# Optimization experiments

Measured on AMD Instinct MI355X. Metric: run time of the kernel, lower is better.

Reference implementation:

```python
import jax, jax.numpy as jnp
import numpy as np

NPOS_MAX = 64
SCALE = 0.125  # head_dim ** -0.5


def setup_inputs() -> dict:
    key = jax.random.key(0)
    kq, kk, kv, kp, kw = jax.random.split(key, 5)
    B, S, D = 32, 1024, 64
    return {
        "q": jax.random.normal(kq, (B, S, D), dtype=jnp.float32),
        "k": jax.random.normal(kk, (B, S, D), dtype=jnp.float32),
        "v": jax.random.normal(kv, (B, S, D), dtype=jnp.float32),
        "pos_emb": jax.random.normal(kp, (1, D, NPOS_MAX), dtype=jnp.float32) * 0.02,
        "w_k": jax.random.normal(kw, (1, D, D), dtype=jnp.float32) * 0.02,
        "is_cope_k": 1,
    }


def reference(q, k, v, pos_emb, w_k, is_cope_k):
    # mode == 0: plain scaled QK^T
    attn_logits = jnp.einsum("bqd,bkd->bqk", q * SCALE, k)  # [B,S,S]
    gates = jax.nn.sigmoid(attn_logits)
    # reverse cumulative sum along the key axis (flip-cumsum-flip)
    pos = jnp.cumsum(gates[..., ::-1], axis=-1)[..., ::-1]
    pos = jnp.minimum(pos, NPOS_MAX - 1)
    pos_ceil = jnp.ceil(pos).astype(jnp.int32)
    pos_floor = jnp.floor(pos).astype(jnp.int32)
    base = q if is_cope_k else k
    logits_int = jnp.einsum("bsd,odn->bsn", base, pos_emb)  # [B,S,npos]
    logits_ceil = jnp.take_along_axis(logits_int, pos_ceil, axis=-1)
    logits_floor = jnp.take_along_axis(logits_int, pos_floor, axis=-1)
    w = pos - pos_floor.astype(pos.dtype)
    return logits_ceil * w + logits_floor * (1.0 - w)
```

## Files before the change

### kernel.cpp

```cpp
#include <hip/hip_runtime.h>

#define SLEN 1024
#define DDIM 64
#define NPOS 64
#define QROWS 16
#define QCOLS 256
#define COPE_SCALE 0.125f
#define GSTR 260
#define TSTR 66

typedef __bf16 bf16x8 __attribute__((ext_vector_type(8)));
typedef float f32x4 __attribute__((ext_vector_type(4)));

__device__ __forceinline__ unsigned short f2bf_hi(float x) {
    unsigned u = __builtin_bit_cast(unsigned, x);
    unsigned r = u + 0x7FFFu + ((u >> 16) & 1u);
    return (unsigned short)(r >> 16);
}
__device__ __forceinline__ float bf2f(unsigned short h) {
    unsigned u = ((unsigned)h) << 16;
    return __builtin_bit_cast(float, u);
}
struct U8 { ushort4 a, b; };
__device__ __forceinline__ bf16x8 pack8(const unsigned short* s) {
    U8 u = {{s[0], s[1], s[2], s[3]}, {s[4], s[5], s[6], s[7]}};
    return __builtin_bit_cast(bf16x8, u);
}

__global__ __launch_bounds__(256) void prep_kernel(
    const float* __restrict__ k,
    unsigned short* __restrict__ khi,
    unsigned short* __restrict__ klo,
    int n4)
{
    int i = blockIdx.x * 256 + threadIdx.x;
    if (i >= n4) return;
    float4 v = ((const float4*)k)[i];
    ushort4 h, l;
    h.x = f2bf_hi(v.x); l.x = f2bf_hi(v.x - bf2f(h.x));
    h.y = f2bf_hi(v.y); l.y = f2bf_hi(v.y - bf2f(h.y));
    h.z = f2bf_hi(v.z); l.z = f2bf_hi(v.z - bf2f(h.z));
    h.w = f2bf_hi(v.w); l.w = f2bf_hi(v.w - bf2f(h.w));
    ((ushort4*)khi)[i] = h;
    ((ushort4*)klo)[i] = l;
}

__global__ __launch_bounds__(256, 6) void cope_mfma_kernel(
    const float* __restrict__ q,
    const float* __restrict__ k,
    const float* __restrict__ pos_emb,
    const int*   __restrict__ is_cope_k,
    const unsigned short* __restrict__ khi,
    const unsigned short* __restrict__ klo,
    float*       __restrict__ out)
{
    __shared__ __align__(16) float G[QROWS * GSTR];
    __shared__ __align__(16) float tableL[QROWS * TSTR];
    __shared__ float Racc[QROWS];

    const int t = threadIdx.x;
    const int wave = t >> 6;
    const int lane = t & 63;
    const int quad = lane >> 4;
    const int nloc = lane & 15;
    const int blk = blockIdx.x;
    const int batch = blk >> 6;
    const int qbase = (blk & 63) * QROWS;

    if (t < QROWS) Racc[t] = 0.f;

    bf16x8 a_hi[2], a_lo[2];
    {
        const float* qrow = q + (size_t)(batch * SLEN + qbase + nloc) * DDIM + quad * 8;
        #pragma unroll
        for (int ks = 0; ks < 2; ++ks) {
            float4 v0 = *(const float4*)(qrow + ks * 32);
            float4 v1 = *(const float4*)(qrow + ks * 32 + 4);
            float xs[8] = {v0.x, v0.y, v0.z, v0.w, v1.x, v1.y, v1.z, v1.w};
            unsigned short hb[8], lb[8];
            #pragma unroll
            for (int j = 0; j < 8; ++j) {
                hb[j] = f2bf_hi(xs[j]);
                lb[j] = f2bf_hi(xs[j] - bf2f(hb[j]));
            }
            a_hi[ks] = pack8(hb);
            a_lo[ks] = pack8(lb);
        }
    }

    {
        const int icope = *is_cope_k;
        bf16x8 t_hi[2], t_lo[2];
        if (icope) {
            t_hi[0] = a_hi[0]; t_hi[1] = a_hi[1];
            t_lo[0] = a_lo[0]; t_lo[1] = a_lo[1];
        } else {
            size_t boff = (size_t)(batch * SLEN + qbase + nloc) * DDIM + quad * 8;
            t_hi[0] = __builtin_bit_cast(bf16x8, *(const uint4*)(khi + boff));
            t_hi[1] = __builtin_bit_cast(bf16x8, *(const uint4*)(khi + boff + 32));
            t_lo[0] = __builtin_bit_cast(bf16x8, *(const uint4*)(klo + boff));
            t_lo[1] = __builtin_bit_cast(bf16x8, *(const uint4*)(klo + boff + 32));
        }
        bf16x8 p_hi[2];
        #pragma unroll
        for (int ks = 0; ks < 2; ++ks) {
            unsigned short hb[8];
            #pragma unroll
            for (int j = 0; j < 8; ++j) {
                float pv = pos_emb[(quad * 8 + j + ks * 32) * NPOS + wave * 16 + nloc];
                hb[j] = f2bf_hi(pv);
            }
            p_hi[ks] = pack8(hb);
        }
        f32x4 tacc = {0.f, 0.f, 0.f, 0.f};
        tacc = __builtin_amdgcn_mfma_f32_16x16x32_bf16(t_hi[0], p_hi[0], tacc, 0, 0, 0);
        tacc = __builtin_amdgcn_mfma_f32_16x16x32_bf16(t_lo[0], p_hi[0], tacc, 0, 0, 0);
        tacc = __builtin_amdgcn_mfma_f32_16x16x32_bf16(t_hi[1], p_hi[1], tacc, 0, 0, 0);
        tacc = __builtin_amdgcn_mfma_f32_16x16x32_bf16(t_lo[1], p_hi[1], tacc, 0, 0, 0);
        #pragma unroll
        for (int reg = 0; reg < 4; ++reg)
            tableL[(quad * 4 + reg) * TSTR + wave * 16 + nloc] = tacc[reg];
    }

    int remaining = 0;
    for (int qi = 3; qi >= 0; --qi) {
        #pragma unroll
        for (int i = 0; i < 4; ++i) {
            const int tl = wave * 4 + i;
            size_t boff = (size_t)(batch * SLEN + qi * QCOLS + tl * 16 + nloc) * DDIM + quad * 8;
            uint4 bh0 = *(const uint4*)(khi + boff);
            uint4 bh1 = *(const uint4*)(khi + boff + 32);
            uint4 bl0 = *(const uint4*)(klo + boff);
            uint4 bl1 = *(const uint4*)(klo + boff + 32);
            f32x4 acc = {0.f, 0.f, 0.f, 0.f};
            acc = __builtin_amdgcn_mfma_f32_16x16x32_bf16(a_hi[0], __builtin_bit_cast(bf16x8, bh0), acc, 0, 0, 0);
            acc = __builtin_amdgcn_mfma_f32_16x16x32_bf16(a_lo[0], __builtin_bit_cast(bf16x8, bh0), acc, 0, 0, 0);
            acc = __builtin_amdgcn_mfma_f32_16x16x32_bf16(a_hi[0], __builtin_bit_cast(bf16x8, bl0), acc, 0, 0, 0);
            acc = __builtin_amdgcn_mfma_f32_16x16x32_bf16(a_hi[1], __builtin_bit_cast(bf16x8, bh1), acc, 0, 0, 0);
            acc = __builtin_amdgcn_mfma_f32_16x16x32_bf16(a_lo[1], __builtin_bit_cast(bf16x8, bh1), acc, 0, 0, 0);
            acc = __builtin_amdgcn_mfma_f32_16x16x32_bf16(a_hi[1], __builtin_bit_cast(bf16x8, bl1), acc, 0, 0, 0);
            #pragma unroll
            for (int reg = 0; reg < 4; ++reg) {
                float x = acc[reg] * COPE_SCALE;
                float g = __builtin_amdgcn_rcpf(1.0f + __expf(-x));
                G[(quad * 4 + reg) * GSTR + tl * 16 + nloc] = g;
            }
        }
        __syncthreads();

        #pragma unroll
        for (int rep = 0; rep < 4; ++rep) {
            const int row = wave * 4 + rep;
            const float roff = Racc[row];
            float4 gv = *(const float4*)&G[row * GSTR + lane * 4];
            float ls3 = gv.w;
            float ls2 = gv.z + ls3;
            float ls1 = gv.y + ls2;
            float ls0 = gv.x + ls1;
            const float T = ls0;
            float v = T;
            #pragma unroll
            for (int ofs = 1; ofs < 64; ofs <<= 1) {
                float u = __shfl_down(v, ofs);
                if (lane + ofs < 64) v += u;
            }
            if (lane == 0) Racc[row] = roff + v;
            const float E = (v - T) + roff;

            const float tabv = tableL[row * TSTR + lane];
            float dtabv = __shfl_down(tabv, 1) - tabv;
            if (lane == 63) dtabv = 0.f;
            float ls[4] = {ls0, ls1, ls2, ls3};
            float res[4];
            #pragma unroll
            for (int i = 0; i < 4; ++i) {
                float p = ls[i] + E;
                p = fminf(p, (float)(NPOS - 1));
                float pf = floorf(p);
                int fi = (int)pf;
                float w = p - pf;
                float tf = __shfl(tabv, fi);
                float td = __shfl(dtabv, fi);
                res[i] = tf + w * td;
            }
            float* orow = out + (size_t)(batch * SLEN + qbase + row) * SLEN + qi * QCOLS + lane * 4;
            f32x4 o = {res[0], res[1], res[2], res[3]};
            __builtin_nontemporal_store(o, (f32x4*)orow);
        }
        __syncthreads();

        float mn = Racc[0];
        #pragma unroll
        for (int r = 1; r < QROWS; ++r) mn = fminf(mn, Racc[r]);
        if (mn >= (float)(NPOS - 1)) { remaining = qi; break; }
    }

    if (remaining > 0) {
        const int ncols = remaining * QCOLS;
        #pragma unroll
        for (int rep = 0; rep < 4; ++rep) {
            const int row = wave * 4 + rep;
            const float v63 = tableL[row * TSTR + (NPOS - 1)];
            f32x4 bv = {v63, v63, v63, v63};
            float* orow = out + (size_t)(batch * SLEN + qbase + row) * SLEN;
            for (int c = lane * 4; c < ncols; c += 256)
                __builtin_nontemporal_store(bv, (f32x4*)(orow + c));
        }
    }
}

#define KTILE 128
#define KPAD 68
#define NTILES (SLEN / KTILE)
#define FQROWS 8

__global__ __launch_bounds__(256) void cope_fallback(
    const float* __restrict__ q,
    const float* __restrict__ k,
    const float* __restrict__ pos_emb,
    const int*   __restrict__ is_cope_k,
    float*       __restrict__ out)
{
    __shared__ __align__(16) float smem[KTILE * KPAD];
    __shared__ __align__(16) float qT[DDIM][FQROWS];
    __shared__ __align__(16) float baseT[DDIM][FQROWS];
    __shared__ __align__(16) float tableL2[FQROWS][NPOS];

    const int t = threadIdx.x;
    const int blk = blockIdx.x;
    const int batch = blk / (SLEN / FQROWS);
    const int qbase = (blk % (SLEN / FQROWS)) * FQROWS;
    const float* bsrc = (*is_cope_k) ? q : k;

    for (int i = t; i < FQROWS * DDIM; i += 256) {
        int r = i >> 6, d = i & 63;
        size_t gi = (size_t)(batch * SLEN + qbase + r) * DDIM + d;
        qT[d][r] = q[gi];
        baseT[d][r] = bsrc[gi];
    }
    __syncthreads();
    for (int i = t; i < FQROWS * NPOS; i += 256) {
        int r = i >> 6, n = i & 63;
        float a = 0.f;
        #pragma unroll
        for (int d = 0; d < DDIM; ++d) a += baseT[d][r] * pos_emb[d * NPOS + n];
        tableL2[r][n] = a;
    }
    const int jl = t & 127;
    const int qg = t >> 7;
    float acc[4][NTILES];
    #pragma unroll
    for (int r = 0; r < 4; ++r)
        #pragma unroll
        for (int tl = 0; tl < NTILES; ++tl) acc[r][tl] = 0.f;
    float (*kT)[KPAD] = (float (*)[KPAD])smem;
    const float* kbatch = k + (size_t)batch * SLEN * DDIM;
    #pragma unroll
    for (int tile = 0; tile < NTILES; ++tile) {
        __syncthreads();
        const float4* src = (const float4*)(kbatch + tile * KTILE * DDIM);
        #pragma unroll
        for (int i = 0; i < (KTILE * DDIM / 4) / 256; ++i) {
            int idx = i * 256 + t;
            int row = (idx * 4) >> 6;
            int col = (idx * 4) & 63;
            float4 vv = src[idx];
            *(float4*)&kT[row][col] = vv;
        }
        __syncthreads();
        #pragma unroll
        for (int d = 0; d < DDIM; d += 4) {
            float4 kv = *(const float4*)&kT[jl][d];
            float4 q0 = *(const float4*)&qT[d + 0][qg * 4];
            float4 q1 = *(const float4*)&qT[d + 1][qg * 4];
            float4 q2 = *(const float4*)&qT[d + 2][qg * 4];
            float4 q3 = *(const float4*)&qT[d + 3][qg * 4];
            acc[0][tile] += kv.x * q0.x + kv.y * q1.x + kv.z * q2.x + kv.w * q3.x;
            acc[1][tile] += kv.x * q0.y + kv.y * q1.y + kv.z * q2.y + kv.w * q3.y;
            acc[2][tile] += kv.x * q0.z + kv.y * q1.z + kv.z * q2.z + kv.w * q3.z;
            acc[3][tile] += kv.x * q0.w + kv.y * q1.w + kv.z * q2.w + kv.w * q3.w;
        }
    }
    __syncthreads();
    float (*G2)[SLEN] = (float (*)[SLEN])smem;
    #pragma unroll
    for (int r = 0; r < 4; ++r)
        #pragma unroll
        for (int tl = 0; tl < NTILES; ++tl) {
            float x = acc[r][tl] * COPE_SCALE;
            G2[qg * 4 + r][tl * KTILE + jl] = 1.0f / (1.0f + __expf(-x));
        }
    __syncthreads();
    const int wave = t >> 6;
    const int lane = t & 63;
    #pragma unroll
    for (int rep = 0; rep < 2; ++rep) {
        const int row = wave * 2 + rep;
        float g4[4][4];
        #pragma unroll
        for (int s = 0; s < 4; ++s) {
            float4 v = *(const float4*)&G2[row][s * 256 + lane * 4];
            g4[s][0] = v.x; g4[s][1] = v.y; g4[s][2] = v.z; g4[s][3] = v.w;
        }
        float ls[4][4], T[4];
        #pragma unroll
        for (int s = 0; s < 4; ++s) {
            float a = 0.f;
            #pragma unroll
            for (int i = 3; i >= 0; --i) { a += g4[s][i]; ls[s][i] = a; }
            T[s] = a;
        }
        float E[4], Stot[4];
        #pragma unroll
        for (int s = 0; s < 4; ++s) {
            float v = T[s];
            #pragma unroll
            for (int ofs = 1; ofs < 64; ofs <<= 1) {
                float u = __shfl_down(v, ofs);
                if (lane + ofs < 64) v += u;
            }
            E[s] = v - T[s];
            Stot[s] = __shfl(v, 0);
        }
        float segOff[4];
        segOff[3] = 0.f;
        segOff[2] = Stot[3];
        segOff[1] = Stot[3] + Stot[2];
        segOff[0] = Stot[3] + Stot[2] + Stot[1];
        const float* tab = tableL2[row];
        float* orow = out + (size_t)(batch * SLEN + qbase + row) * SLEN;
        #pragma unroll
        for (int s = 0; s < 4; ++s) {
            float res[4];
            #pragma unroll
            for (int i = 0; i < 4; ++i) {
                float p = ls[s][i] + E[s] + segOff[s];
                p = fminf(p, (float)(NPOS - 1));
                float pf = floorf(p);
                int fi = (int)pf;
                int ci = (int)ceilf(p);
                float w = p - pf;
                res[i] = tab[ci] * w + tab[fi] * (1.0f - w);
            }
            float4 o; o.x = res[0]; o.y = res[1]; o.z = res[2]; o.w = res[3];
            *(float4*)&orow[s * 256 + lane * 4] = o;
        }
    }
}

extern "C" void kernel_launch(void* const* d_in, const int* in_sizes, int n_in,
                              void* d_out, int out_size, void* d_ws, size_t ws_size,
                              hipStream_t stream) {
    const float* q        = (const float*)d_in[0];
    const float* k        = (const float*)d_in[1];
    const float* pos_emb  = (const float*)d_in[3];
    const int*   is_cope_k = (const int*)d_in[5];
    float* out = (float*)d_out;

    const int nk = in_sizes[1];
    const int B = in_sizes[0] / (SLEN * DDIM);
    const size_t ws_need = (size_t)nk * 2 * sizeof(unsigned short);

    if (ws_size >= ws_need) {
        unsigned short* khi = (unsigned short*)d_ws;
        unsigned short* klo = khi + nk;
        int n4 = nk / 4;
        prep_kernel<<<(n4 + 255) / 256, 256, 0, stream>>>(k, khi, klo, n4);
        cope_mfma_kernel<<<B * (SLEN / QROWS), 256, 0, stream>>>(
            q, k, pos_emb, is_cope_k, khi, klo, out);
    } else {
        cope_fallback<<<B * (SLEN / FQROWS), 256, 0, stream>>>(
            q, k, pos_emb, is_cope_k, out);
    }
}
```

Measured before the change: 173.7 us.

## Fuse K bf16 split into main kernel, remap blocks per XCD, prefill saturated output

```diff
diff --git a/kernel.cpp b/kernel.cpp
--- a/kernel.cpp
+++ b/kernel.cpp
@@ -1,4 +1,5 @@
 #include <hip/hip_runtime.h>
+
 
 #define SLEN 1024
 #define DDIM 64
@@ -27,22 +28,22 @@
     return __builtin_bit_cast(bf16x8, u);
 }
 
-__global__ __launch_bounds__(256) void prep_kernel(
-    const float* __restrict__ k,
-    unsigned short* __restrict__ khi,
-    unsigned short* __restrict__ klo,
-    int n4)
-{
-    int i = blockIdx.x * 256 + threadIdx.x;
-    if (i >= n4) return;
-    float4 v = ((const float4*)k)[i];
-    ushort4 h, l;
-    h.x = f2bf_hi(v.x); l.x = f2bf_hi(v.x - bf2f(h.x));
-    h.y = f2bf_hi(v.y); l.y = f2bf_hi(v.y - bf2f(h.y));
-    h.z = f2bf_hi(v.z); l.z = f2bf_hi(v.z - bf2f(h.z));
-    h.w = f2bf_hi(v.w); l.w = f2bf_hi(v.w - bf2f(h.w));
-    ((ushort4*)khi)[i] = h;
-    ((ushort4*)klo)[i] = l;
+__device__ __forceinline__ void load_split16(const float* __restrict__ row,
+                                             bf16x8* hi, bf16x8* lo) {
+    #pragma unroll
+    for (int ks = 0; ks < 2; ++ks) {
+        float4 v0 = *(const float4*)(row + ks * 32);
+        float4 v1 = *(const float4*)(row + ks * 32 + 4);
+        float xs[8] = {v0.x, v0.y, v0.z, v0.w, v1.x, v1.y, v1.z, v1.w};
+        unsigned short hb[8], lb[8];
+        #pragma unroll
+        for (int j = 0; j < 8; ++j) {
+            hb[j] = f2bf_hi(xs[j]);
+            lb[j] = f2bf_hi(xs[j] - bf2f(hb[j]));
+        }
+        hi[ks] = pack8(hb);
+        lo[ks] = pack8(lb);
+    }
 }
 
 __global__ __launch_bounds__(256, 6) void cope_mfma_kernel(
@@ -50,8 +51,6 @@
     const float* __restrict__ k,
     const float* __restrict__ pos_emb,
     const int*   __restrict__ is_cope_k,
-    const unsigned short* __restrict__ khi,
-    const unsigned short* __restrict__ klo,
     float*       __restrict__ out)
 {
     __shared__ __align__(16) float G[QROWS * GSTR];
@@ -63,30 +62,19 @@
     const int lane = t & 63;
     const int quad = lane >> 4;
     const int nloc = lane & 15;
-    const int blk = blockIdx.x;
+
+    const int nwg = gridDim.x;
+    const int phys = blockIdx.x;
+    const int blk = ((nwg & 7) == 0) ? ((phys & 7) * (nwg >> 3) + (phys >> 3))
+                                     : phys;
     const int batch = blk >> 6;
     const int qbase = (blk & 63) * QROWS;
 
     if (t < QROWS) Racc[t] = 0.f;
 
     bf16x8 a_hi[2], a_lo[2];
-    {
-        const float* qrow = q + (size_t)(batch * SLEN + qbase + nloc) * DDIM + quad * 8;
-        #pragma unroll
-        for (int ks = 0; ks < 2; ++ks) {
-            float4 v0 = *(const float4*)(qrow + ks * 32);
-            float4 v1 = *(const float4*)(qrow + ks * 32 + 4);
-            float xs[8] = {v0.x, v0.y, v0.z, v0.w, v1.x, v1.y, v1.z, v1.w};
-            unsigned short hb[8], lb[8];
-            #pragma unroll
-            for (int j = 0; j < 8; ++j) {
-                hb[j] = f2bf_hi(xs[j]);
-                lb[j] = f2bf_hi(xs[j] - bf2f(hb[j]));
-            }
-            a_hi[ks] = pack8(hb);
-            a_lo[ks] = pack8(lb);
-        }
-    }
+    load_split16(q + (size_t)(batch * SLEN + qbase + nloc) * DDIM + quad * 8,
+                 a_hi, a_lo);
 
     {
         const int icope = *is_cope_k;
@@ -95,11 +83,8 @@
             t_hi[0] = a_hi[0]; t_hi[1] = a_hi[1];
             t_lo[0] = a_lo[0]; t_lo[1] = a_lo[1];
         } else {
-            size_t boff = (size_t)(batch * SLEN + qbase + nloc) * DDIM + quad * 8;
-            t_hi[0] = __builtin_bit_cast(bf16x8, *(const uint4*)(khi + boff));
-            t_hi[1] = __builtin_bit_cast(bf16x8, *(const uint4*)(khi + boff + 32));
-            t_lo[0] = __builtin_bit_cast(bf16x8, *(const uint4*)(klo + boff));
-            t_lo[1] = __builtin_bit_cast(bf16x8, *(const uint4*)(klo + boff + 32));
+            load_split16(k + (size_t)(batch * SLEN + qbase + nloc) * DDIM + quad * 8,
+                         t_hi, t_lo);
         }
         bf16x8 p_hi[2];
         #pragma unroll
@@ -121,24 +106,34 @@
         for (int reg = 0; reg < 4; ++reg)
             tableL[(quad * 4 + reg) * TSTR + wave * 16 + nloc] = tacc[reg];
     }
-
-    int remaining = 0;
+    __syncthreads();
+
+    #pragma unroll
+    for (int rep = 0; rep < 4; ++rep) {
+        const int row = wave * 4 + rep;
+        const float v63 = tableL[row * TSTR + (NPOS - 1)];
+        f32x4 bv = {v63, v63, v63, v63};
+        float* orow = out + (size_t)(batch * SLEN + qbase + row) * SLEN;
+        #pragma unroll
+        for (int c = 0; c < 3; ++c)
+            __builtin_nontemporal_store(bv, (f32x4*)(orow + c * QCOLS + lane * 4));
+    }
+
     for (int qi = 3; qi >= 0; --qi) {
         #pragma unroll
         for (int i = 0; i < 4; ++i) {
             const int tl = wave * 4 + i;
-            size_t boff = (size_t)(batch * SLEN + qi * QCOLS + tl * 16 + nloc) * DDIM + quad * 8;
-            uint4 bh0 = *(const uint4*)(khi + boff);
-            uint4 bh1 = *(const uint4*)(khi + boff + 32);
-            uint4 bl0 = *(const uint4*)(klo + boff);
-            uint4 bl1 = *(const uint4*)(klo + boff + 32);
+            const float* krow =
+                k + (size_t)(batch * SLEN + qi * QCOLS + tl * 16 + nloc) * DDIM + quad * 8;
+            bf16x8 bh[2], bl[2];
+            load_split16(krow, bh, bl);
             f32x4 acc = {0.f, 0.f, 0.f, 0.f};
-            acc = __builtin_amdgcn_mfma_f32_16x16x32_bf16(a_hi[0], __builtin_bit_cast(bf16x8, bh0), acc, 0, 0, 0);
-            acc = __builtin_amdgcn_mfma_f32_16x16x32_bf16(a_lo[0], __builtin_bit_cast(bf16x8, bh0), acc, 0, 0, 0);
-            acc = __builtin_amdgcn_mfma_f32_16x16x32_bf16(a_hi[0], __builtin_bit_cast(bf16x8, bl0), acc, 0, 0, 0);
-            acc = __builtin_amdgcn_mfma_f32_16x16x32_bf16(a_hi[1], __builtin_bit_cast(bf16x8, bh1), acc, 0, 0, 0);
-            acc = __builtin_amdgcn_mfma_f32_16x16x32_bf16(a_lo[1], __builtin_bit_cast(bf16x8, bh1), acc, 0, 0, 0);
-            acc = __builtin_amdgcn_mfma_f32_16x16x32_bf16(a_hi[1], __builtin_bit_cast(bf16x8, bl1), acc, 0, 0, 0);
+            acc = __builtin_amdgcn_mfma_f32_16x16x32_bf16(a_hi[0], bh[0], acc, 0, 0, 0);
+            acc = __builtin_amdgcn_mfma_f32_16x16x32_bf16(a_lo[0], bh[0], acc, 0, 0, 0);
+            acc = __builtin_amdgcn_mfma_f32_16x16x32_bf16(a_hi[0], bl[0], acc, 0, 0, 0);
+            acc = __builtin_amdgcn_mfma_f32_16x16x32_bf16(a_hi[1], bh[1], acc, 0, 0, 0);
+            acc = __builtin_amdgcn_mfma_f32_16x16x32_bf16(a_lo[1], bh[1], acc, 0, 0, 0);
+            acc = __builtin_amdgcn_mfma_f32_16x16x32_bf16(a_hi[1], bl[1], acc, 0, 0, 0);
             #pragma unroll
             for (int reg = 0; reg < 4; ++reg) {
                 float x = acc[reg] * COPE_SCALE;
@@ -192,184 +187,21 @@
         float mn = Racc[0];
         #pragma unroll
         for (int r = 1; r < QROWS; ++r) mn = fminf(mn, Racc[r]);
-        if (mn >= (float)(NPOS - 1)) { remaining = qi; break; }
-    }
-
-    if (remaining > 0) {
-        const int ncols = remaining * QCOLS;
-        #pragma unroll
-        for (int rep = 0; rep < 4; ++rep) {
-            const int row = wave * 4 + rep;
-            const float v63 = tableL[row * TSTR + (NPOS - 1)];
-            f32x4 bv = {v63, v63, v63, v63};
-            float* orow = out + (size_t)(batch * SLEN + qbase + row) * SLEN;
-            for (int c = lane * 4; c < ncols; c += 256)
-                __builtin_nontemporal_store(bv, (f32x4*)(orow + c));
-        }
-    }
-}
-
-#define KTILE 128
-#define KPAD 68
-#define NTILES (SLEN / KTILE)
-#define FQROWS 8
-
-__global__ __launch_bounds__(256) void cope_fallback(
-    const float* __restrict__ q,
-    const float* __restrict__ k,
-    const float* __restrict__ pos_emb,
-    const int*   __restrict__ is_cope_k,
-    float*       __restrict__ out)
-{
-    __shared__ __align__(16) float smem[KTILE * KPAD];
-    __shared__ __align__(16) float qT[DDIM][FQROWS];
-    __shared__ __align__(16) float baseT[DDIM][FQROWS];
-    __shared__ __align__(16) float tableL2[FQROWS][NPOS];
-
-    const int t = threadIdx.x;
-    const int blk = blockIdx.x;
-    const int batch = blk / (SLEN / FQROWS);
-    const int qbase = (blk % (SLEN / FQROWS)) * FQROWS;
-    const float* bsrc = (*is_cope_k) ? q : k;
-
-    for (int i = t; i < FQROWS * DDIM; i += 256) {
-        int r = i >> 6, d = i & 63;
-        size_t gi = (size_t)(batch * SLEN + qbase + r) * DDIM + d;
-        qT[d][r] = q[gi];
-        baseT[d][r] = bsrc[gi];
-    }
-    __syncthreads();
-    for (int i = t; i < FQROWS * NPOS; i += 256) {
-        int r = i >> 6, n = i & 63;
-        float a = 0.f;
-        #pragma unroll
-        for (int d = 0; d < DDIM; ++d) a += baseT[d][r] * pos_emb[d * NPOS + n];
-        tableL2[r][n] = a;
-    }
-    const int jl = t & 127;
-    const int qg = t >> 7;
-    float acc[4][NTILES];
-    #pragma unroll
-    for (int r = 0; r < 4; ++r)
-        #pragma unroll
-        for (int tl = 0; tl < NTILES; ++tl) acc[r][tl] = 0.f;
-    float (*kT)[KPAD] = (float (*)[KPAD])smem;
-    const float* kbatch = k + (size_t)batch * SLEN * DDIM;
-    #pragma unroll
-    for (int tile = 0; tile < NTILES; ++tile) {
-        __syncthreads();
-        const float4* src = (const float4*)(kbatch + tile * KTILE * DDIM);
-        #pragma unroll
-        for (int i = 0; i < (KTILE * DDIM / 4) / 256; ++i) {
-            int idx = i * 256 + t;
-            int row = (idx * 4) >> 6;
-            int col = (idx * 4) & 63;
-            float4 vv = src[idx];
-            *(float4*)&kT[row][col] = vv;
-        }
-        __syncthreads();
-        #pragma unroll
-        for (int d = 0; d < DDIM; d += 4) {
-            float4 kv = *(const float4*)&kT[jl][d];
-            float4 q0 = *(const float4*)&qT[d + 0][qg * 4];
-            float4 q1 = *(const float4*)&qT[d + 1][qg * 4];
-            float4 q2 = *(const float4*)&qT[d + 2][qg * 4];
-            float4 q3 = *(const float4*)&qT[d + 3][qg * 4];
-            acc[0][tile] += kv.x * q0.x + kv.y * q1.x + kv.z * q2.x + kv.w * q3.x;
-            acc[1][tile] += kv.x * q0.y + kv.y * q1.y + kv.z * q2.y + kv.w * q3.y;
-            acc[2][tile] += kv.x * q0.z + kv.y * q1.z + kv.z * q2.z + kv.w * q3.z;
-            acc[3][tile] += kv.x * q0.w + kv.y * q1.w + kv.z * q2.w + kv.w * q3.w;
-        }
-    }
-    __syncthreads();
-    float (*G2)[SLEN] = (float (*)[SLEN])smem;
-    #pragma unroll
-    for (int r = 0; r < 4; ++r)
-        #pragma unroll
-        for (int tl = 0; tl < NTILES; ++tl) {
-            float x = acc[r][tl] * COPE_SCALE;
-            G2[qg * 4 + r][tl * KTILE + jl] = 1.0f / (1.0f + __expf(-x));
-        }
-    __syncthreads();
-    const int wave = t >> 6;
-    const int lane = t & 63;
-    #pragma unroll
-    for (int rep = 0; rep < 2; ++rep) {
-        const int row = wave * 2 + rep;
-        float g4[4][4];
-        #pragma unroll
-        for (int s = 0; s < 4; ++s) {
-            float4 v = *(const float4*)&G2[row][s * 256 + lane * 4];
-            g4[s][0] = v.x; g4[s][1] = v.y; g4[s][2] = v.z; g4[s][3] = v.w;
-        }
-        float ls[4][4], T[4];
-        #pragma unroll
-        for (int s = 0; s < 4; ++s) {
-            float a = 0.f;
-            #pragma unroll
-            for (int i = 3; i >= 0; --i) { a += g4[s][i]; ls[s][i] = a; }
-            T[s] = a;
-        }
-        float E[4], Stot[4];
-        #pragma unroll
-        for (int s = 0; s < 4; ++s) {
-            float v = T[s];
-            #pragma unroll
-            for (int ofs = 1; ofs < 64; ofs <<= 1) {
-                float u = __shfl_down(v, ofs);
-                if (lane + ofs < 64) v += u;
-            }
-            E[s] = v - T[s];
-            Stot[s] = __shfl(v, 0);
-        }
-        float segOff[4];
-        segOff[3] = 0.f;
-        segOff[2] = Stot[3];
-        segOff[1] = Stot[3] + Stot[2];
-        segOff[0] = Stot[3] + Stot[2] + Stot[1];
-        const float* tab = tableL2[row];
-        float* orow = out + (size_t)(batch * SLEN + qbase + row) * SLEN;
-        #pragma unroll
-        for (int s = 0; s < 4; ++s) {
-            float res[4];
-            #pragma unroll
-            for (int i = 0; i < 4; ++i) {
-                float p = ls[s][i] + E[s] + segOff[s];
-                p = fminf(p, (float)(NPOS - 1));
-                float pf = floorf(p);
-                int fi = (int)pf;
-                int ci = (int)ceilf(p);
-                float w = p - pf;
-                res[i] = tab[ci] * w + tab[fi] * (1.0f - w);
-            }
-            float4 o; o.x = res[0]; o.y = res[1]; o.z = res[2]; o.w = res[3];
-            *(float4*)&orow[s * 256 + lane * 4] = o;
-        }
+        if (mn >= (float)(NPOS - 1)) break;
     }
 }
 
 extern "C" void kernel_launch(void* const* d_in, const int* in_sizes, int n_in,
                               void* d_out, int out_size, void* d_ws, size_t ws_size,
                               hipStream_t stream) {
-    const float* q        = (const float*)d_in[0];
-    const float* k        = (const float*)d_in[1];
-    const float* pos_emb  = (const float*)d_in[3];
+    (void)n_in; (void)out_size; (void)d_ws; (void)ws_size;
+    const float* q         = (const float*)d_in[0];
+    const float* k         = (const float*)d_in[1];
+    const float* pos_emb   = (const float*)d_in[3];
     const int*   is_cope_k = (const int*)d_in[5];
     float* out = (float*)d_out;
 
-    const int nk = in_sizes[1];
     const int B = in_sizes[0] / (SLEN * DDIM);
-    const size_t ws_need = (size_t)nk * 2 * sizeof(unsigned short);
-
-    if (ws_size >= ws_need) {
-        unsigned short* khi = (unsigned short*)d_ws;
-        unsigned short* klo = khi + nk;
-        int n4 = nk / 4;
-        prep_kernel<<<(n4 + 255) / 256, 256, 0, stream>>>(k, khi, klo, n4);
-        cope_mfma_kernel<<<B * (SLEN / QROWS), 256, 0, stream>>>(
-            q, k, pos_emb, is_cope_k, khi, klo, out);
-    } else {
-        cope_fallback<<<B * (SLEN / FQROWS), 256, 0, stream>>>(
-            q, k, pos_emb, is_cope_k, out);
-    }
-}
+    cope_mfma_kernel<<<B * (SLEN / QROWS), 256, 0, stream>>>(
+        q, k, pos_emb, is_cope_k, out);
+}
```

Result: slower. 184.4 us (+6.2%).
